# Kernel tuning notes

Hardware: AMD Instinct MI355X
Metric: run time of the kernel (lower is better)

## Reference

```python
import jax, jax.numpy as jnp
import numpy as np
from jax import lax

V, D, P, C = 151936, 1024, 64, 28
B, S = 1, 1024
EPS = 1.1920929e-07  # torch.finfo(float32).eps, used by nn.RMSNorm(eps=None)


def setup_inputs() -> dict:
    key = jax.random.key(0)
    ks = jax.random.split(key, 10)
    return {
        "tokens": jax.random.randint(ks[0], (B, S), 0, V),
        "embed_table": jax.random.normal(ks[1], (V, D), jnp.float32) * 0.02,
        "plane_proj_w": jax.random.normal(ks[2], (C, 2 * P, D), jnp.float32) * (1.0 / np.sqrt(D)),
        "back_proj_w": jax.random.normal(ks[3], (C, D, 2 * P), jnp.float32) * 0.02,
        "base_angles": jax.random.normal(ks[4], (C, P), jnp.float32) * 0.1,
        "angle_gen_w": jax.random.normal(ks[5], (P, D), jnp.float32) * 0.01,
        "scales": jnp.ones((C, D), jnp.float32),
        "shifts": jnp.zeros((C, D), jnp.float32),
        "norm_w": jnp.ones((C, D), jnp.float32),
        "decay_param": jnp.float32(0.9),
        "gate_w": jax.random.normal(ks[6], (D, D), jnp.float32) * 0.02,
        "out_norm_w": jnp.ones((D,), jnp.float32),
        "lm_head_w": jax.random.normal(ks[7], (V, D), jnp.float32) * 0.02,
    }


def _rms_norm(v, w):
    return v * lax.rsqrt(jnp.mean(v * v, axis=-1, keepdims=True) + EPS) * w


def _causal_mix(x, decay_param, gate_w):
    # state_t = d*state_{t-1} + (1-d)*x_t, causal EMA over sequence
    d = jax.nn.sigmoid(decay_param)
    def step(s, xt):
        s = d * s + (1.0 - d) * xt
        return s, s
    _, ys = lax.scan(step, jnp.zeros(x.shape[::2], x.dtype)[0:0].sum(0) + jnp.zeros((x.shape[0], x.shape[2]), x.dtype), jnp.swapaxes(x, 0, 1))
    causal = jnp.swapaxes(ys, 0, 1)  # [B,S,D]
    return x + causal @ gate_w.T


def reference(tokens, embed_table, plane_proj_w, back_proj_w, base_angles,
              angle_gen_w, scales, shifts, norm_w, decay_param, gate_w,
              out_norm_w, lm_head_w):
    x = embed_table[tokens].astype(jnp.float32)  # [B,S,D]
    n_cycles = scales.shape[0]
    for i in range(n_cycles):
        # input-dependent angle offset (detached in the original)
        extra = x.mean(axis=1) @ angle_gen_w.T          # [B,P]
        angles = base_angles[i] + lax.stop_gradient(extra.mean(axis=0)) * 0.1
        if i % 4 == 0:
            x = _causal_mix(x, decay_param, gate_w)
        # learned-plane rotation
        proj = x @ plane_proj_w[i].T                     # [B,S,2P]
        n = proj.shape[-1] // 2
        a, b = proj[..., :n], proj[..., n:]
        ca, sa = jnp.cos(angles), jnp.sin(angles)
        rot = jnp.concatenate([a * ca - b * sa, a * sa + b * ca], axis=-1)
        x_rot = x + rot @ back_proj_w[i].T
        x_act = jax.nn.silu(x_rot * scales[i] + shifts[i])
        x = x + _rms_norm(x_act - x, norm_w[i])
    x = _rms_norm(x, out_norm_w)
    return x @ lm_head_w.T  # [B,S,V]
```

## Files before the change

kernel.cpp:

```cpp
#include <hip/hip_runtime.h>

typedef __attribute__((ext_vector_type(4))) float f32x4;
typedef __attribute__((ext_vector_type(8))) short bf16x8;
typedef unsigned short u16;
typedef unsigned int u32;
typedef __attribute__((ext_vector_type(4))) unsigned short u16x4;

#define EPS 1.1920929e-07f
#define S 1024
#define D 1024
#define NV 151936
#define NCYC 28
#define SMEM_BYTES 49152

__device__ __forceinline__ u16 f2bf(float f) {
  u32 u = __float_as_uint(f);
  return (u16)((u + 0x7fffu + ((u >> 16) & 1u)) >> 16);
}
__device__ __forceinline__ float bf2f(u16 h) {
  return __uint_as_float((u32)h << 16);
}
struct bfpair { u16 h, l; };
__device__ __forceinline__ bfpair split_bf(float v) {
  bfpair r;
  r.h = f2bf(v);
  r.l = f2bf(v - bf2f(r.h));
  return r;
}

__device__ __forceinline__ void gl16(const void* g, void* s) {
  __builtin_amdgcn_global_load_lds((const __attribute__((address_space(1))) u32*)g,
                                   (__attribute__((address_space(3))) u32*)s, 16, 0, 0);
}

__device__ __forceinline__ float block_sum256(float v, float* sbuf) {
  #pragma unroll
  for (int off = 32; off; off >>= 1) v += __shfl_down(v, off);
  int lane = threadIdx.x & 63, w = threadIdx.x >> 6;
  __syncthreads();
  if (lane == 0) sbuf[w] = v;
  __syncthreads();
  return sbuf[0] + sbuf[1] + sbuf[2] + sbuf[3];
}

__device__ void cvt2_range(const float* __restrict__ src, u16* __restrict__ dh,
                           u16* __restrict__ dl, size_t n4, int blkbase, int nblk) {
  for (size_t i = (size_t)(blockIdx.x - blkbase) * 256 + threadIdx.x; i < n4;
       i += (size_t)nblk * 256) {
    f32x4 v = ((const f32x4*)src)[i];
    u16x4 oh, ol;
    #pragma unroll
    for (int e = 0; e < 4; ++e) { bfpair p = split_bf(v[e]); oh[e] = p.h; ol[e] = p.l; }
    ((u16x4*)dh)[i] = oh;
    ((u16x4*)dl)[i] = ol;
  }
}

__device__ void side_cvt(const float* __restrict__ src, u16* __restrict__ dst,
                         int chunk, int blkbase) {
  if (!src) return;
  const size_t n4 = (size_t)NV * D / 4;
  const size_t per = (n4 + (size_t)(NCYC * 3) - 1) / (size_t)(NCYC * 3);
  size_t lo = (size_t)chunk * per;
  size_t hi = lo + per;
  if (hi > n4) hi = n4;
  const size_t nb = (size_t)(gridDim.x - blkbase);
  for (size_t i = lo + (size_t)(blockIdx.x - blkbase) * 256 + threadIdx.x; i < hi;
       i += nb * 256) {
    f32x4 v = ((const f32x4*)src)[i];
    u16x4 o;
    #pragma unroll
    for (int e = 0; e < 4; ++e) o[e] = f2bf(v[e]);
    ((u16x4*)dst)[i] = o;
  }
}


__device__ void gather_phase(const int* tokens, const float* embed,
                             float* x, u16* xh, u16* xl, float* cp) {
  const int t = threadIdx.x;
  f32x4 creg = 0.f;
  for (int rr = 0; rr < 4; ++rr) {
    int s = blockIdx.x * 4 + rr;
    int tok = tokens[s];
    f32x4 v = ((const f32x4*)(embed + (size_t)tok * D))[t];
    u16x4 oh, ol;
    #pragma unroll
    for (int e = 0; e < 4; ++e) { bfpair p = split_bf(v[e]); oh[e] = p.h; ol[e] = p.l; }
    ((f32x4*)(x + (size_t)s * D))[t] = v;
    ((u16x4*)(xh + (size_t)s * D))[t] = oh;
    ((u16x4*)(xl + (size_t)s * D))[t] = ol;
    creg += v;
  }
  *(f32x4*)(cp + (size_t)blockIdx.x * D + t * 4) = creg;
}

template <bool CADD>
__device__ void gemm64_dbuf(char* smem, const u16* Ah_, const u16* Al_,
                            const u16* Bh_, const u16* Bl_, int K,
                            float* xout, u16* xho, u16* xlo, float* Cout) {
  const int t = threadIdx.x;
  u16* Ash = (u16*)smem;
  u16* Asl = Ash + 8192;
  u16* Bsh = Asl + 8192;
  u16* Bsl = Bsh + 8192;
  const int wave = t >> 6, lane = t & 63;
  const int fr = lane & 15, kb = lane >> 4;
  const int sr = t >> 3, skc = (t & 7) << 3;
  const int sswz = skc ^ ((sr & 7) << 3);
  const int m0 = (blockIdx.x >> 4) * 64, n0 = (blockIdx.x & 15) * 64;
  f32x4 acc[4];
  #pragma unroll
  for (int j = 0; j < 4; ++j) acc[j] = 0.f;

  auto stage = [&](int buf, int k0) {
    #pragma unroll
    for (int it = 0; it < 2; ++it) {
      int r = it * 32 + sr;
      size_t ga = (size_t)(m0 + r) * K + k0 + sswz;
      size_t gb = (size_t)(n0 + r) * K + k0 + sswz;
      int so = buf * 4096 + r * 64 + skc;
      gl16(Ah_ + ga, Ash + so);
      gl16(Al_ + ga, Asl + so);
      gl16(Bh_ + gb, Bsh + so);
      gl16(Bl_ + gb, Bsl + so);
    }
  };
  const int nt = K >> 6;
  stage(0, 0);
  __syncthreads();
  for (int kt = 0; kt < nt; ++kt) {
    const int cur = kt & 1;
    if (kt + 1 < nt) stage(cur ^ 1, (kt + 1) << 6);
    const int co = cur * 4096;
    #pragma unroll
    for (int ks = 0; ks < 2; ++ks) {
      const int cphys = (ks * 32 + kb * 8) ^ ((fr & 7) << 3);
      int oa = co + (wave * 16 + fr) * 64 + cphys;
      bf16x8 ah = *(const bf16x8*)&Ash[oa];
      bf16x8 al = *(const bf16x8*)&Asl[oa];
      #pragma unroll
      for (int j = 0; j < 4; ++j) {
        int ob = co + (j * 16 + fr) * 64 + cphys;
        bf16x8 bh = *(const bf16x8*)&Bsh[ob];
        bf16x8 bl = *(const bf16x8*)&Bsl[ob];
        acc[j] = __builtin_amdgcn_mfma_f32_16x16x32_bf16(ah, bh, acc[j], 0, 0, 0);
        acc[j] = __builtin_amdgcn_mfma_f32_16x16x32_bf16(ah, bl, acc[j], 0, 0, 0);
        acc[j] = __builtin_amdgcn_mfma_f32_16x16x32_bf16(al, bh, acc[j], 0, 0, 0);
      }
    }
    __syncthreads();
  }
  #pragma unroll
  for (int j = 0; j < 4; ++j)
    #pragma unroll
    for (int rg = 0; rg < 4; ++rg) {
      int m = m0 + wave * 16 + kb * 4 + rg;
      int n = n0 + j * 16 + fr;
      if (CADD) {
        float v = xout[(size_t)m * D + n] + acc[j][rg];
        xout[(size_t)m * D + n] = v;
        bfpair p = split_bf(v);
        xho[(size_t)m * D + n] = p.h;
        xlo[(size_t)m * D + n] = p.l;
      } else {
        Cout[(size_t)m * D + n] = acc[j][rg];
      }
    }
}

__device__ void causal_phase(char* smem, const float* x, u16* Rh, u16* Rl,
                             float dec, int G) {
  const int t = threadIdx.x;
  for (int tile = blockIdx.x; tile < 256; tile += G) {
    int s0 = (tile >> 4) * 64, d0 = (tile & 15) * 64;
    float (*tl)[64] = (float(*)[64])smem;
    for (int idx = t; idx < 159 * 64; idx += 256) {
      int rr = idx >> 6, c = idx & 63;
      int gs = s0 - 95 + rr;
      tl[rr][c] = (gs >= 0) ? x[(size_t)gs * D + d0 + c] : 0.f;
    }
    __syncthreads();
    int c = t & 63, r0 = t >> 6;
    for (int rr = r0; rr < 64; rr += 4) {
      float acc = 0.f, w = 1.f - dec;
      int base = rr + 95;
      #pragma unroll 8
      for (int j = 0; j < 96; ++j) { acc += w * tl[base - j][c]; w *= dec; }
      bfpair p = split_bf(acc);
      Rh[(size_t)(s0 + rr) * D + d0 + c] = p.h;
      Rl[(size_t)(s0 + rr) * D + d0 + c] = p.l;
    }
    __syncthreads();
  }
}

__device__ void proj_phase(char* smem, const u16* xh, const u16* xl,
                           const u16* Bh_, const u16* Bl_, float* pacc) {
  const int t = threadIdx.x;
  const int mt = blockIdx.x & 15, kq = blockIdx.x >> 4;
  const int m0 = mt * 64;
  const int k0 = kq * 64;
  u16* Ash = (u16*)smem;
  u16* Asl = Ash + 4096;
  u16* Bsh = Asl + 4096;
  u16* Bsl = Bsh + 8192;
  const int wave = t >> 6, lane = t & 63;
  const int fr = lane & 15, kb = lane >> 4;
  const int sr = t >> 3, skc = (t & 7) << 3;
  const int sswz = skc ^ ((sr & 7) << 3);
  f32x4 acc[8];
  #pragma unroll
  for (int j = 0; j < 8; ++j) acc[j] = 0.f;

  #pragma unroll
  for (int it = 0; it < 2; ++it) {
    int r = it * 32 + sr;
    size_t ga = (size_t)(m0 + r) * D + k0 + sswz;
    gl16(xh + ga, Ash + r * 64 + skc);
    gl16(xl + ga, Asl + r * 64 + skc);
  }
  #pragma unroll
  for (int it = 0; it < 4; ++it) {
    int r = it * 32 + sr;
    size_t gb = (size_t)r * D + k0 + sswz;
    gl16(Bh_ + gb, Bsh + r * 64 + skc);
    gl16(Bl_ + gb, Bsl + r * 64 + skc);
  }
  __syncthreads();
  #pragma unroll
  for (int ks = 0; ks < 2; ++ks) {
    const int cphys = (ks * 32 + kb * 8) ^ ((fr & 7) << 3);
    int oa = (wave * 16 + fr) * 64 + cphys;
    bf16x8 ah = *(const bf16x8*)&Ash[oa];
    bf16x8 al = *(const bf16x8*)&Asl[oa];
    #pragma unroll
    for (int j = 0; j < 8; ++j) {
      int ob = (j * 16 + fr) * 64 + cphys;
      bf16x8 bh = *(const bf16x8*)&Bsh[ob];
      bf16x8 bl = *(const bf16x8*)&Bsl[ob];
      acc[j] = __builtin_amdgcn_mfma_f32_16x16x32_bf16(ah, bh, acc[j], 0, 0, 0);
      acc[j] = __builtin_amdgcn_mfma_f32_16x16x32_bf16(ah, bl, acc[j], 0, 0, 0);
      acc[j] = __builtin_amdgcn_mfma_f32_16x16x32_bf16(al, bh, acc[j], 0, 0, 0);
    }
  }
  float* pb = pacc + (size_t)blockIdx.x * 64 * 128;
  #pragma unroll
  for (int j = 0; j < 8; ++j)
    #pragma unroll
    for (int rg = 0; rg < 4; ++rg) {
      int ml = wave * 16 + kb * 4 + rg;
      pb[ml * 128 + j * 16 + fr] = acc[j][rg];
    }
}

__device__ void angles_all(float* colsum, const float* cp, const float* agw,
                           const float* bang_i, float* trig) {
  const int t = threadIdx.x;
  f32x4 acc = 0.f;
  for (int b = 0; b < 256; ++b)
    acc += *(const f32x4*)(cp + (size_t)b * D + t * 4);
  *(f32x4*)&colsum[t * 4] = acc;
  __syncthreads();
  const int wave = t >> 6, lane = t & 63;
  for (int pp = 0; pp < 16; ++pp) {
    int p = wave * 16 + pp;
    float sum = 0.f;
    #pragma unroll
    for (int q = 0; q < 16; ++q) {
      int d = lane + q * 64;
      sum += colsum[d] * agw[p * D + d];
    }
    #pragma unroll
    for (int off = 32; off; off >>= 1) sum += __shfl_down(sum, off);
    if (lane == 0) {
      float ang = bang_i[p] + 0.1f * (sum * (1.f / (float)S));
      trig[p] = cosf(ang);
      trig[64 + p] = sinf(ang);
    }
  }
}

__device__ void epilogue_phase(float* sbuf, float* x, u16* xh, u16* xl,
                               const float* Rf, const float* scale,
                               const float* shift, const float* nw, float* cp,
                               const float* onorm, u16* xn, int last) {
  const int t = threadIdx.x;
  f32x4 sc = *(const f32x4*)(scale + t * 4);
  f32x4 sh = *(const f32x4*)(shift + t * 4);
  f32x4 nwv = *(const f32x4*)(nw + t * 4);
  f32x4 creg = 0.f;
  for (int rr = 0; rr < 4; ++rr) {
    int s = blockIdx.x * 4 + rr;
    f32x4 xv = *(const f32x4*)(x + (size_t)s * D + t * 4);
    f32x4 rv = *(const f32x4*)(Rf + (size_t)s * D + t * 4);
    float y[4], ss = 0.f;
    #pragma unroll
    for (int c = 0; c < 4; ++c) {
      float xr = xv[c] + rv[c];
      float tt = xr * sc[c] + sh[c];
      float act = tt / (1.f + expf(-tt));
      y[c] = act - xv[c];
      ss += y[c] * y[c];
    }
    float total = block_sum256(ss, sbuf);
    float inv = rsqrtf(total * (1.f / (float)D) + EPS);
    f32x4 o;
    u16x4 oh, ol;
    #pragma unroll
    for (int c = 0; c < 4; ++c) {
      o[c] = xv[c] + y[c] * inv * nwv[c];
      bfpair p = split_bf(o[c]);
      oh[c] = p.h;
      ol[c] = p.l;
      creg[c] += o[c];
    }
    *(f32x4*)(x + (size_t)s * D + t * 4) = o;
    *(u16x4*)(xh + (size_t)s * D + t * 4) = oh;
    *(u16x4*)(xl + (size_t)s * D + t * 4) = ol;
    if (last) {
      float s2 = o[0]*o[0] + o[1]*o[1] + o[2]*o[2] + o[3]*o[3];
      float tot2 = block_sum256(s2, sbuf);
      float inv2 = rsqrtf(tot2 * (1.f / (float)D) + EPS);
      f32x4 ow = *(const f32x4*)(onorm + t * 4);
      u16x4 on;
      #pragma unroll
      for (int c = 0; c < 4; ++c) on[c] = f2bf(o[c] * inv2 * ow[c]);
      *(u16x4*)(xn + (size_t)s * D + t * 4) = on;
    }
  }
  *(f32x4*)(cp + (size_t)blockIdx.x * D + t * 4) = creg;
}

__global__ __launch_bounds__(256) void fb_gather(const int* tokens, const float* embed,
                                                 float* x, u16* xh, u16* xl, float* cp,
                                                 const float* gatew, u16* gh, u16* gl,
                                                 const float* Wp, u16* Wph, u16* Wpl,
                                                 const float* Wb, u16* Wbh, u16* Wbl) {
  if (blockIdx.x < 256) {
    gather_phase(tokens, embed, x, xh, xl, cp);
  } else if (blockIdx.x < 384) {
    cvt2_range(gatew, gh, gl, (size_t)D * D / 4, 256, 128);
  } else if (blockIdx.x < 576) {
    cvt2_range(Wp, Wph, Wpl, (size_t)NCYC * 128 * D / 4, 384, 192);
  } else {
    cvt2_range(Wb, Wbh, Wbl, (size_t)NCYC * 128 * D / 4, 576, 192);
  }
}
__global__ __launch_bounds__(256) void fb_causal(const float* x, u16* Rh, u16* Rl,
                                                 const float* decay) {
  __shared__ __align__(16) char sm[40704];
  causal_phase(sm, x, Rh, Rl, 1.f / (1.f + expf(-decay[0])), gridDim.x);
}
__global__ __launch_bounds__(256) void fb_gate(const u16* Rh, const u16* Rl,
                                               const u16* gh, const u16* gl,
                                               float* x, u16* xh, u16* xl) {
  __shared__ __align__(16) char sm[65536];
  gemm64_dbuf<true>(sm, Rh, Rl, gh, gl, 1024, x, xh, xl, nullptr);
}
__global__ __launch_bounds__(256) void fb_proj(const u16* xh, const u16* xl,
                                               const u16* Wph, const u16* Wpl,
                                               const float* cp, const float* agw,
                                               const float* bang_i,
                                               float* pacc, float* trig,
                                               const float* lmw, u16* lm_bf, int chunk) {
  __shared__ __align__(16) char sm[SMEM_BYTES];
  if (blockIdx.x < 256) proj_phase(sm, xh, xl, Wph, Wpl, pacc);
  else if (blockIdx.x == 256) angles_all((float*)sm, cp, agw, bang_i, trig);
  else side_cvt(lmw, lm_bf, chunk, 257);
}

__global__ __launch_bounds__(256) void fb_back(const float* __restrict__ pacc,
                                               const float* __restrict__ trig,
                                               const u16* __restrict__ Bh_,
                                               const u16* __restrict__ Bl_,
                                               float* __restrict__ Rf,
                                               const float* lmw, u16* lm_bf, int chunk) {
  __shared__ u16 Ash[64 * 128];
  __shared__ u16 Asl[64 * 128];
  __shared__ u16 Bsh[64 * 64];
  __shared__ u16 Bsl[64 * 64];
  if (blockIdx.x >= 256) { side_cvt(lmw, lm_bf, chunk, 256); return; }
  const int t = threadIdx.x;
  const int tile = blockIdx.x;
  const int mt = tile >> 4;
  const int m0 = mt * 64, n0 = (tile & 15) * 64;
  const int wave = t >> 6, lane = t & 63;
  const int fr = lane & 15, kb = lane >> 4;
  const int sr = t >> 3, skc = (t & 7) << 3;
  const int sswz = skc ^ ((sr & 7) << 3);

  #pragma unroll
  for (int ri = 0; ri < 2; ++ri) {
    int r = ri * 32 + sr;
    int pdst = skc ^ ((r & 7) << 3);
    f32x4 a0 = 0.f, a1 = 0.f, b0 = 0.f, b1 = 0.f;
    #pragma unroll
    for (int kq = 0; kq < 16; ++kq) {
      const float* pk = pacc + ((size_t)(kq * 16 + mt) * 64 + r) * 128;
      a0 += *(const f32x4*)(pk + skc);
      a1 += *(const f32x4*)(pk + skc + 4);
      b0 += *(const f32x4*)(pk + 64 + skc);
      b1 += *(const f32x4*)(pk + 64 + skc + 4);
    }
    #pragma unroll
    for (int kh = 0; kh < 2; ++kh) {
      u16 hbuf[8], lbuf[8];
      #pragma unroll
      for (int j = 0; j < 8; ++j) {
        float av = (j < 4) ? a0[j & 3] : a1[j & 3];
        float bv = (j < 4) ? b0[j & 3] : b1[j & 3];
        float ca = trig[skc + j], sa = trig[64 + skc + j];
        float v = (kh == 0) ? (av * ca - bv * sa) : (av * sa + bv * ca);
        bfpair p = split_bf(v);
        hbuf[j] = p.h;
        lbuf[j] = p.l;
      }
      int so = r * 128 + kh * 64 + pdst;
      *(bf16x8*)&Ash[so] = *(bf16x8*)hbuf;
      *(bf16x8*)&Asl[so] = *(bf16x8*)lbuf;
    }
  }
  __syncthreads();

  f32x4 acc[4];
  #pragma unroll
  for (int j = 0; j < 4; ++j) acc[j] = 0.f;

  for (int kt = 0; kt < 2; ++kt) {
    int k0 = kt * 64;
    #pragma unroll
    for (int it = 0; it < 2; ++it) {
      int r = it * 32 + sr;
      size_t gb = (size_t)(n0 + r) * 128 + k0 + sswz;
      gl16(Bh_ + gb, Bsh + r * 64 + skc);
      gl16(Bl_ + gb, Bsl + r * 64 + skc);
    }
    __syncthreads();
    #pragma unroll
    for (int ks = 0; ks < 2; ++ks) {
      const int w = (ks * 32 + kb * 8) ^ ((fr & 7) << 3);
      int oa = (wave * 16 + fr) * 128 + k0 + w;
      bf16x8 ah = *(const bf16x8*)&Ash[oa];
      bf16x8 al = *(const bf16x8*)&Asl[oa];
      #pragma unroll
      for (int j = 0; j < 4; ++j) {
        int ob = (j * 16 + fr) * 64 + w;
        bf16x8 bh = *(const bf16x8*)&Bsh[ob];
        bf16x8 bl = *(const bf16x8*)&Bsl[ob];
        acc[j] = __builtin_amdgcn_mfma_f32_16x16x32_bf16(ah, bh, acc[j], 0, 0, 0);
        acc[j] = __builtin_amdgcn_mfma_f32_16x16x32_bf16(ah, bl, acc[j], 0, 0, 0);
        acc[j] = __builtin_amdgcn_mfma_f32_16x16x32_bf16(al, bh, acc[j], 0, 0, 0);
      }
    }
    __syncthreads();
  }
  #pragma unroll
  for (int j = 0; j < 4; ++j)
    #pragma unroll
    for (int rg = 0; rg < 4; ++rg) {
      int m = m0 + wave * 16 + kb * 4 + rg;
      int n = n0 + j * 16 + fr;
      Rf[(size_t)m * D + n] = acc[j][rg];
    }
}

__global__ __launch_bounds__(256) void fb_epi(float* x, u16* xh, u16* xl, const float* Rf,
                                              const float* scale, const float* shift,
                                              const float* nw, float* cp,
                                              const float* onorm, u16* xn, int last,
                                              const float* lmw, u16* lm_bf, int chunk) {
  __shared__ float sbuf[4];
  if (blockIdx.x < 256)
    epilogue_phase(sbuf, x, xh, xl, Rf, scale, shift, nw, cp, onorm, xn, last);
  else
    side_cvt(lmw, lm_bf, chunk, 256);
}

template <bool PRECONV>
__global__ __launch_bounds__(256) void k_lm(const u16* __restrict__ A,
                                            const void* __restrict__ Wsrc,
                                            float* __restrict__ out) {
  __shared__ u16 As[128 * 64];
  __shared__ u16 Bs[128 * 64];
  const int bid = blockIdx.x;
  const int lid = (bid & 7) * 1187 + (bid >> 3);
  const int m0 = (lid & 7) * 128;
  const int n0 = (lid >> 3) * 128;
  const int t = threadIdx.x;
  const int wave = t >> 6, lane = t & 63;
  const int wm = (wave >> 1) * 64, wn = (wave & 1) * 64;
  const int fr = lane & 15, kb = lane >> 4;
  const int sr = t >> 3, skc = (t & 7) << 3;
  const int sswz = skc ^ ((sr & 7) << 3);
  const u16* Wb16 = (const u16*)Wsrc;
  const float* Wf = (const float*)Wsrc;
  f32x4 acc[4][4];
  #pragma unroll
  for (int i = 0; i < 4; ++i)
    #pragma unroll
    for (int j = 0; j < 4; ++j) acc[i][j] = 0.f;

  for (int k0 = 0; k0 < D; k0 += 64) {
    #pragma unroll
    for (int it = 0; it < 4; ++it) {
      int r = it * 32 + sr;
      gl16(A + (size_t)(m0 + r) * D + k0 + sswz, As + r * 64 + skc);
    }
    if (PRECONV) {
      #pragma unroll
      for (int it = 0; it < 4; ++it) {
        int r = it * 32 + sr;
        gl16(Wb16 + (size_t)(n0 + r) * D + k0 + sswz, Bs + r * 64 + skc);
      }
    } else {
      #pragma unroll
      for (int it = 0; it < 4; ++it) {
        int r = it * 32 + sr;
        const float* src = Wf + (size_t)(n0 + r) * D + k0 + sswz;
        f32x4 v0 = *(const f32x4*)src;
        f32x4 v1 = *(const f32x4*)(src + 4);
        u16 h[8];
        #pragma unroll
        for (int e = 0; e < 4; ++e) { h[e] = f2bf(v0[e]); h[e + 4] = f2bf(v1[e]); }
        *(bf16x8*)&Bs[r * 64 + skc] = *(bf16x8*)h;
      }
    }
    __syncthreads();
    #pragma unroll
    for (int ks = 0; ks < 2; ++ks) {
      const int cphys = (ks * 32 + kb * 8) ^ ((fr & 7) << 3);
      bf16x8 a[4], b[4];
      #pragma unroll
      for (int i = 0; i < 4; ++i) a[i] = *(const bf16x8*)&As[(wm + i * 16 + fr) * 64 + cphys];
      #pragma unroll
      for (int j = 0; j < 4; ++j) b[j] = *(const bf16x8*)&Bs[(wn + j * 16 + fr) * 64 + cphys];
      #pragma unroll
      for (int i = 0; i < 4; ++i)
        #pragma unroll
        for (int j = 0; j < 4; ++j)
          acc[i][j] = __builtin_amdgcn_mfma_f32_16x16x32_bf16(a[i], b[j], acc[i][j], 0, 0, 0);
    }
    __syncthreads();
  }
  #pragma unroll
  for (int i = 0; i < 4; ++i)
    #pragma unroll
    for (int j = 0; j < 4; ++j)
      #pragma unroll
      for (int rg = 0; rg < 4; ++rg) {
        int m = m0 + wm + i * 16 + kb * 4 + rg;
        int n = n0 + wn + j * 16 + fr;
        out[(size_t)m * NV + n] = acc[i][j][rg];
      }
}

extern "C" void kernel_launch(void* const* d_in, const int* in_sizes, int n_in,
                              void* d_out, int out_size, void* d_ws, size_t ws_size,
                              hipStream_t stream) {
  const int* tokens = (const int*)d_in[0];
  const float* embed = (const float*)d_in[1];
  const float* Wp = (const float*)d_in[2];
  const float* Wb = (const float*)d_in[3];
  const float* bang = (const float*)d_in[4];
  const float* agw = (const float*)d_in[5];
  const float* scales = (const float*)d_in[6];
  const float* shifts = (const float*)d_in[7];
  const float* normw = (const float*)d_in[8];
  const float* decay = (const float*)d_in[9];
  const float* gatew = (const float*)d_in[10];
  const float* onorm = (const float*)d_in[11];
  const float* lmw = (const float*)d_in[12];
  float* out = (float*)d_out;

  char* ws = (char*)d_ws;
  const size_t MB = 1u << 20;
  float* x = (float*)ws;
  u16* xh = (u16*)(ws + 4 * MB);
  u16* xl = (u16*)(ws + 6 * MB);
  float* Rf = (float*)(ws + 8 * MB);
  u16* Rh = (u16*)(ws + 12 * MB);
  u16* Rl = (u16*)(ws + 14 * MB);
  float* trig = (float*)(ws + 16 * MB);
  float* cp = (float*)(ws + 17 * MB);
  u16* xn = (u16*)(ws + 20 * MB);
  u16* gate_h = (u16*)(ws + 22 * MB);
  u16* gate_l = (u16*)(ws + 24 * MB);
  u16* Wp_h = (u16*)(ws + 26 * MB);
  u16* Wp_l = (u16*)(ws + 33 * MB);
  u16* Wb_h = (u16*)(ws + 40 * MB);
  u16* Wb_l = (u16*)(ws + 47 * MB);
  float* pacc = (float*)(ws + 54 * MB);
  u16* lm_bf = (u16*)(ws + 62 * MB);

  const size_t lm_elems = (size_t)NV * D;
  bool preconv = ws_size >= 62 * MB + lm_elems * 2;
  const float* side_src = preconv ? lmw : nullptr;
  u16* side_dst = preconv ? lm_bf : nullptr;
  const int gproj = preconv ? 385 : 257;
  const int gside = preconv ? 384 : 256;

  fb_gather<<<768, 256, 0, stream>>>(tokens, embed, x, xh, xl, cp,
                                     gatew, gate_h, gate_l,
                                     Wp, Wp_h, Wp_l, Wb, Wb_h, Wb_l);
  for (int i = 0; i < NCYC; ++i) {
    const u16* Wph = Wp_h + (size_t)i * 128 * D;
    const u16* Wpl = Wp_l + (size_t)i * 128 * D;
    const u16* Wbh = Wb_h + (size_t)i * 128 * D;
    const u16* Wbl = Wb_l + (size_t)i * 128 * D;
    if ((i & 3) == 0) {
      fb_causal<<<256, 256, 0, stream>>>(x, Rh, Rl, decay);
      fb_gate<<<256, 256, 0, stream>>>(Rh, Rl, gate_h, gate_l, x, xh, xl);
    }
    fb_proj<<<gproj, 256, 0, stream>>>(xh, xl, Wph, Wpl, cp, agw, bang + i * 64,
                                       pacc, trig, side_src, side_dst, i * 3);
    fb_back<<<gside, 256, 0, stream>>>(pacc, trig, Wbh, Wbl, Rf,
                                       side_src, side_dst, i * 3 + 1);
    fb_epi<<<gside, 256, 0, stream>>>(x, xh, xl, Rf, scales + i * D, shifts + i * D,
                                      normw + i * D, cp, onorm, xn,
                                      (i == NCYC - 1) ? 1 : 0,
                                      side_src, side_dst, i * 3 + 2);
  }

  if (preconv)
    k_lm<true><<<9496, 256, 0, stream>>>(xn, lm_bf, out);
  else
    k_lm<false><<<9496, 256, 0, stream>>>(xn, lmw, out);
}
```

Baseline: 2.773 ms.

## Fuse back-projection into epilogue using fp32 FMA and drop Wb bf16 split

Merges the back-projection GEMM and the silu/RMSNorm epilogue into one kernel per cycle. Each block handles 4 rows, rotates the reduced projection in shared memory, and computes the 4x1024 back-projection with scalar fp32 FMAs that read Wb directly in fp32. This removes the Rf round-trip, one launch per cycle, and the upfront hi/lo bf16 conversion of Wb. The side lm_head conversion is spread over two kernels per cycle instead of three. The cost is that every block now rereads the full 512KB Wb slice per cycle (256 blocks) with non-coalesced strided loads instead of MFMA.

Result: no change. 2.767 ms (median of 2 runs) (-0.2%).

```diff
diff --git a/kernel.cpp b/kernel.cpp
--- a/kernel.cpp
+++ b/kernel.cpp
@@ -60,7 +60,7 @@
                          int chunk, int blkbase) {
   if (!src) return;
   const size_t n4 = (size_t)NV * D / 4;
-  const size_t per = (n4 + (size_t)(NCYC * 3) - 1) / (size_t)(NCYC * 3);
+  const size_t per = (n4 + (size_t)(NCYC * 2) - 1) / (size_t)(NCYC * 2);
   size_t lo = (size_t)chunk * per;
   size_t hi = lo + per;
   if (hi > n4) hi = n4;
@@ -281,70 +281,16 @@
   }
 }
 
-__device__ void epilogue_phase(float* sbuf, float* x, u16* xh, u16* xl,
-                               const float* Rf, const float* scale,
-                               const float* shift, const float* nw, float* cp,
-                               const float* onorm, u16* xn, int last) {
-  const int t = threadIdx.x;
-  f32x4 sc = *(const f32x4*)(scale + t * 4);
-  f32x4 sh = *(const f32x4*)(shift + t * 4);
-  f32x4 nwv = *(const f32x4*)(nw + t * 4);
-  f32x4 creg = 0.f;
-  for (int rr = 0; rr < 4; ++rr) {
-    int s = blockIdx.x * 4 + rr;
-    f32x4 xv = *(const f32x4*)(x + (size_t)s * D + t * 4);
-    f32x4 rv = *(const f32x4*)(Rf + (size_t)s * D + t * 4);
-    float y[4], ss = 0.f;
-    #pragma unroll
-    for (int c = 0; c < 4; ++c) {
-      float xr = xv[c] + rv[c];
-      float tt = xr * sc[c] + sh[c];
-      float act = tt / (1.f + expf(-tt));
-      y[c] = act - xv[c];
-      ss += y[c] * y[c];
-    }
-    float total = block_sum256(ss, sbuf);
-    float inv = rsqrtf(total * (1.f / (float)D) + EPS);
-    f32x4 o;
-    u16x4 oh, ol;
-    #pragma unroll
-    for (int c = 0; c < 4; ++c) {
-      o[c] = xv[c] + y[c] * inv * nwv[c];
-      bfpair p = split_bf(o[c]);
-      oh[c] = p.h;
-      ol[c] = p.l;
-      creg[c] += o[c];
-    }
-    *(f32x4*)(x + (size_t)s * D + t * 4) = o;
-    *(u16x4*)(xh + (size_t)s * D + t * 4) = oh;
-    *(u16x4*)(xl + (size_t)s * D + t * 4) = ol;
-    if (last) {
-      float s2 = o[0]*o[0] + o[1]*o[1] + o[2]*o[2] + o[3]*o[3];
-      float tot2 = block_sum256(s2, sbuf);
-      float inv2 = rsqrtf(tot2 * (1.f / (float)D) + EPS);
-      f32x4 ow = *(const f32x4*)(onorm + t * 4);
-      u16x4 on;
-      #pragma unroll
-      for (int c = 0; c < 4; ++c) on[c] = f2bf(o[c] * inv2 * ow[c]);
-      *(u16x4*)(xn + (size_t)s * D + t * 4) = on;
-    }
-  }
-  *(f32x4*)(cp + (size_t)blockIdx.x * D + t * 4) = creg;
-}
-
 __global__ __launch_bounds__(256) void fb_gather(const int* tokens, const float* embed,
                                                  float* x, u16* xh, u16* xl, float* cp,
                                                  const float* gatew, u16* gh, u16* gl,
-                                                 const float* Wp, u16* Wph, u16* Wpl,
-                                                 const float* Wb, u16* Wbh, u16* Wbl) {
+                                                 const float* Wp, u16* Wph, u16* Wpl) {
   if (blockIdx.x < 256) {
     gather_phase(tokens, embed, x, xh, xl, cp);
   } else if (blockIdx.x < 384) {
     cvt2_range(gatew, gh, gl, (size_t)D * D / 4, 256, 128);
-  } else if (blockIdx.x < 576) {
+  } else {
     cvt2_range(Wp, Wph, Wpl, (size_t)NCYC * 128 * D / 4, 384, 192);
-  } else {
-    cvt2_range(Wb, Wbh, Wbl, (size_t)NCYC * 128 * D / 4, 576, 192);
   }
 }
 __global__ __launch_bounds__(256) void fb_causal(const float* x, u16* Rh, u16* Rl,
@@ -370,111 +316,135 @@
   else side_cvt(lmw, lm_bf, chunk, 257);
 }
 
-__global__ __launch_bounds__(256) void fb_back(const float* __restrict__ pacc,
-                                               const float* __restrict__ trig,
-                                               const u16* __restrict__ Bh_,
-                                               const u16* __restrict__ Bl_,
-                                               float* __restrict__ Rf,
-                                               const float* lmw, u16* lm_bf, int chunk) {
-  __shared__ u16 Ash[64 * 128];
-  __shared__ u16 Asl[64 * 128];
-  __shared__ u16 Bsh[64 * 64];
-  __shared__ u16 Bsl[64 * 64];
+__global__ __launch_bounds__(256) void fb_epiback(
+    const float* __restrict__ pacc, const float* __restrict__ trig,
+    const float* __restrict__ Wbf,
+    float* __restrict__ x, u16* __restrict__ xh, u16* __restrict__ xl,
+    float* __restrict__ cp, const float* __restrict__ scale,
+    const float* __restrict__ shift, const float* __restrict__ nw,
+    const float* __restrict__ onorm, u16* __restrict__ xn, int last,
+    const float* lmw, u16* lm_bf, int chunk) {
+  __shared__ float praw[4][128];
+  __shared__ float Arot[4][128];
+  __shared__ float sbuf[4];
   if (blockIdx.x >= 256) { side_cvt(lmw, lm_bf, chunk, 256); return; }
   const int t = threadIdx.x;
-  const int tile = blockIdx.x;
-  const int mt = tile >> 4;
-  const int m0 = mt * 64, n0 = (tile & 15) * 64;
-  const int wave = t >> 6, lane = t & 63;
-  const int fr = lane & 15, kb = lane >> 4;
-  const int sr = t >> 3, skc = (t & 7) << 3;
-  const int sswz = skc ^ ((sr & 7) << 3);
-
-  #pragma unroll
-  for (int ri = 0; ri < 2; ++ri) {
-    int r = ri * 32 + sr;
-    int pdst = skc ^ ((r & 7) << 3);
-    f32x4 a0 = 0.f, a1 = 0.f, b0 = 0.f, b1 = 0.f;
-    #pragma unroll
-    for (int kq = 0; kq < 16; ++kq) {
-      const float* pk = pacc + ((size_t)(kq * 16 + mt) * 64 + r) * 128;
-      a0 += *(const f32x4*)(pk + skc);
-      a1 += *(const f32x4*)(pk + skc + 4);
-      b0 += *(const f32x4*)(pk + 64 + skc);
-      b1 += *(const f32x4*)(pk + 64 + skc + 4);
-    }
-    #pragma unroll
-    for (int kh = 0; kh < 2; ++kh) {
-      u16 hbuf[8], lbuf[8];
-      #pragma unroll
-      for (int j = 0; j < 8; ++j) {
-        float av = (j < 4) ? a0[j & 3] : a1[j & 3];
-        float bv = (j < 4) ? b0[j & 3] : b1[j & 3];
-        float ca = trig[skc + j], sa = trig[64 + skc + j];
-        float v = (kh == 0) ? (av * ca - bv * sa) : (av * sa + bv * ca);
-        bfpair p = split_bf(v);
-        hbuf[j] = p.h;
-        lbuf[j] = p.l;
+  const int b = blockIdx.x;
+  const int s0 = b * 4;
+  const int mt = s0 >> 6;
+  const int r64b = s0 & 63;
+
+  #pragma unroll
+  for (int ii = 0; ii < 2; ++ii) {
+    int idx = t + ii * 256;
+    int e = idx >> 7, c = idx & 127;
+    float v = 0.f;
+    #pragma unroll
+    for (int kq = 0; kq < 16; ++kq)
+      v += pacc[((size_t)(kq * 16 + mt) * 64 + r64b + e) * 128 + c];
+    praw[e][c] = v;
+  }
+  __syncthreads();
+  #pragma unroll
+  for (int ii = 0; ii < 2; ++ii) {
+    int idx = t + ii * 256;
+    int e = idx >> 7, c = idx & 127;
+    int p = c & 63;
+    float a = praw[e][p], bb = praw[e][64 + p];
+    float ca = trig[p], sa = trig[64 + p];
+    Arot[e][c] = (c < 64) ? (a * ca - bb * sa) : (a * sa + bb * ca);
+  }
+  __syncthreads();
+
+  float acc[4][4];
+  #pragma unroll
+  for (int e = 0; e < 4; ++e)
+    #pragma unroll
+    for (int q = 0; q < 4; ++q) acc[e][q] = 0.f;
+  const float* wr0 = Wbf + (size_t)t * 128;
+  for (int k = 0; k < 128; k += 4) {
+    f32x4 a0 = *(const f32x4*)&Arot[0][k];
+    f32x4 a1 = *(const f32x4*)&Arot[1][k];
+    f32x4 a2 = *(const f32x4*)&Arot[2][k];
+    f32x4 a3 = *(const f32x4*)&Arot[3][k];
+    #pragma unroll
+    for (int q = 0; q < 4; ++q) {
+      f32x4 w4 = *(const f32x4*)(wr0 + (size_t)q * 256 * 128 + k);
+      #pragma unroll
+      for (int u = 0; u < 4; ++u) {
+        acc[0][q] += a0[u] * w4[u];
+        acc[1][q] += a1[u] * w4[u];
+        acc[2][q] += a2[u] * w4[u];
+        acc[3][q] += a3[u] * w4[u];
       }
-      int so = r * 128 + kh * 64 + pdst;
-      *(bf16x8*)&Ash[so] = *(bf16x8*)hbuf;
-      *(bf16x8*)&Asl[so] = *(bf16x8*)lbuf;
-    }
-  }
-  __syncthreads();
-
-  f32x4 acc[4];
-  #pragma unroll
-  for (int j = 0; j < 4; ++j) acc[j] = 0.f;
-
-  for (int kt = 0; kt < 2; ++kt) {
-    int k0 = kt * 64;
-    #pragma unroll
-    for (int it = 0; it < 2; ++it) {
-      int r = it * 32 + sr;
-      size_t gb = (size_t)(n0 + r) * 128 + k0 + sswz;
-      gl16(Bh_ + gb, Bsh + r * 64 + skc);
-      gl16(Bl_ + gb, Bsl + r * 64 + skc);
-    }
-    __syncthreads();
-    #pragma unroll
-    for (int ks = 0; ks < 2; ++ks) {
-      const int w = (ks * 32 + kb * 8) ^ ((fr & 7) << 3);
-      int oa = (wave * 16 + fr) * 128 + k0 + w;
-      bf16x8 ah = *(const bf16x8*)&Ash[oa];
-      bf16x8 al = *(const bf16x8*)&Asl[oa];
-      #pragma unroll
-      for (int j = 0; j < 4; ++j) {
-        int ob = (j * 16 + fr) * 64 + w;
-        bf16x8 bh = *(const bf16x8*)&Bsh[ob];
-        bf16x8 bl = *(const bf16x8*)&Bsl[ob];
-        acc[j] = __builtin_amdgcn_mfma_f32_16x16x32_bf16(ah, bh, acc[j], 0, 0, 0);
-        acc[j] = __builtin_amdgcn_mfma_f32_16x16x32_bf16(ah, bl, acc[j], 0, 0, 0);
-        acc[j] = __builtin_amdgcn_mfma_f32_16x16x32_bf16(al, bh, acc[j], 0, 0, 0);
-      }
-    }
-    __syncthreads();
-  }
-  #pragma unroll
-  for (int j = 0; j < 4; ++j)
-    #pragma unroll
-    for (int rg = 0; rg < 4; ++rg) {
-      int m = m0 + wave * 16 + kb * 4 + rg;
-      int n = n0 + j * 16 + fr;
-      Rf[(size_t)m * D + n] = acc[j][rg];
-    }
-}
-
-__global__ __launch_bounds__(256) void fb_epi(float* x, u16* xh, u16* xl, const float* Rf,
-                                              const float* scale, const float* shift,
-                                              const float* nw, float* cp,
-                                              const float* onorm, u16* xn, int last,
-                                              const float* lmw, u16* lm_bf, int chunk) {
-  __shared__ float sbuf[4];
-  if (blockIdx.x < 256)
-    epilogue_phase(sbuf, x, xh, xl, Rf, scale, shift, nw, cp, onorm, xn, last);
-  else
-    side_cvt(lmw, lm_bf, chunk, 256);
+    }
+  }
+  float xv[4][4], y[4][4];
+  float ssp[4] = {0.f, 0.f, 0.f, 0.f};
+  #pragma unroll
+  for (int q = 0; q < 4; ++q) {
+    int n = t + q * 256;
+    float scv = scale[n], shv = shift[n];
+    #pragma unroll
+    for (int e = 0; e < 4; ++e) {
+      float xvv = x[(size_t)(s0 + e) * D + n];
+      float tt = (xvv + acc[e][q]) * scv + shv;
+      float act = tt / (1.f + expf(-tt));
+      float yy = act - xvv;
+      xv[e][q] = xvv;
+      y[e][q] = yy;
+      ssp[e] += yy * yy;
+    }
+  }
+
+  float inv_[4];
+  #pragma unroll
+  for (int e = 0; e < 4; ++e) {
+    float tot = block_sum256(ssp[e], sbuf);
+    inv_[e] = rsqrtf(tot * (1.f / (float)D) + EPS);
+  }
+
+  float o_[4][4];
+  #pragma unroll
+  for (int q = 0; q < 4; ++q) {
+    int n = t + q * 256;
+    float nwv = nw[n];
+    float csum = 0.f;
+    #pragma unroll
+    for (int e = 0; e < 4; ++e) {
+      float o = xv[e][q] + y[e][q] * inv_[e] * nwv;
+      o_[e][q] = o;
+      bfpair p = split_bf(o);
+      size_t gi = (size_t)(s0 + e) * D + n;
+      x[gi] = o;
+      xh[gi] = p.h;
+      xl[gi] = p.l;
+      csum += o;
+    }
+    cp[(size_t)b * D + n] = csum;
+  }
+
+  if (last) {
+    float s2p[4] = {0.f, 0.f, 0.f, 0.f};
+    #pragma unroll
+    for (int q = 0; q < 4; ++q)
+      #pragma unroll
+      for (int e = 0; e < 4; ++e) s2p[e] += o_[e][q] * o_[e][q];
+    float inv2[4];
+    #pragma unroll
+    for (int e = 0; e < 4; ++e) {
+      float tot2 = block_sum256(s2p[e], sbuf);
+      inv2[e] = rsqrtf(tot2 * (1.f / (float)D) + EPS);
+    }
+    #pragma unroll
+    for (int q = 0; q < 4; ++q) {
+      int n = t + q * 256;
+      float ow = onorm[n];
+      #pragma unroll
+      for (int e = 0; e < 4; ++e)
+        xn[(size_t)(s0 + e) * D + n] = f2bf(o_[e][q] * inv2[e] * ow);
+    }
+  }
 }
 
 template <bool PRECONV>
@@ -578,7 +548,6 @@
   float* x = (float*)ws;
   u16* xh = (u16*)(ws + 4 * MB);
   u16* xl = (u16*)(ws + 6 * MB);
-  float* Rf = (float*)(ws + 8 * MB);
   u16* Rh = (u16*)(ws + 12 * MB);
   u16* Rl = (u16*)(ws + 14 * MB);
   float* trig = (float*)(ws + 16 * MB);
@@ -588,8 +557,6 @@
   u16* gate_l = (u16*)(ws + 24 * MB);
   u16* Wp_h = (u16*)(ws + 26 * MB);
   u16* Wp_l = (u16*)(ws + 33 * MB);
-  u16* Wb_h = (u16*)(ws + 40 * MB);
-  u16* Wb_l = (u16*)(ws + 47 * MB);
   float* pacc = (float*)(ws + 54 * MB);
   u16* lm_bf = (u16*)(ws + 62 * MB);
 
@@ -600,26 +567,22 @@
   const int gproj = preconv ? 385 : 257;
   const int gside = preconv ? 384 : 256;
 
-  fb_gather<<<768, 256, 0, stream>>>(tokens, embed, x, xh, xl, cp,
-                                     gatew, gate_h, gate_l,
-                                     Wp, Wp_h, Wp_l, Wb, Wb_h, Wb_l);
+  fb_gather<<<576, 256, 0, stream>>>(tokens, embed, x, xh, xl, cp,
+                                     gatew, gate_h, gate_l, Wp, Wp_h, Wp_l);
   for (int i = 0; i < NCYC; ++i) {
     const u16* Wph = Wp_h + (size_t)i * 128 * D;
     const u16* Wpl = Wp_l + (size_t)i * 128 * D;
-    const u16* Wbh = Wb_h + (size_t)i * 128 * D;
-    const u16* Wbl = Wb_l + (size_t)i * 128 * D;
+    const float* Wbf = Wb + (size_t)i * D * 128;
     if ((i & 3) == 0) {
       fb_causal<<<256, 256, 0, stream>>>(x, Rh, Rl, decay);
       fb_gate<<<256, 256, 0, stream>>>(Rh, Rl, gate_h, gate_l, x, xh, xl);
     }
     fb_proj<<<gproj, 256, 0, stream>>>(xh, xl, Wph, Wpl, cp, agw, bang + i * 64,
-                                       pacc, trig, side_src, side_dst, i * 3);
-    fb_back<<<gside, 256, 0, stream>>>(pacc, trig, Wbh, Wbl, Rf,
-                                       side_src, side_dst, i * 3 + 1);
-    fb_epi<<<gside, 256, 0, stream>>>(x, xh, xl, Rf, scales + i * D, shifts + i * D,
-                                      normw + i * D, cp, onorm, xn,
-                                      (i == NCYC - 1) ? 1 : 0,
-                                      side_src, side_dst, i * 3 + 2);
+                                       pacc, trig, side_src, side_dst, i * 2);
+    fb_epiback<<<gside, 256, 0, stream>>>(pacc, trig, Wbf, x, xh, xl, cp,
+                                          scales + i * D, shifts + i * D, normw + i * D,
+                                          onorm, xn, (i == NCYC - 1) ? 1 : 0,
+                                          side_src, side_dst, i * 2 + 1);
   }
 
   if (preconv)
```
